# Performance work log

Measured on AMD Instinct MI355X. Metric: run time of the kernel, lower is better.

The kernel has to match this reference:

```python
import jax, jax.numpy as jnp
import numpy as np

D_MODEL = 1024
D_HID = D_MODEL // 4
N_EXPERTS = 64
TOP_K = 2


def setup_inputs() -> dict:
    key = jax.random.key(0)
    k_x, k_w1, k_b1, k_w2, k_b2 = jax.random.split(key, 5)
    # torch Linear default init: U(-1/sqrt(fan_in), 1/sqrt(fan_in))
    s1 = 1.0 / np.sqrt(D_MODEL)
    s2 = 1.0 / np.sqrt(D_HID)
    return {
        "x": jax.random.normal(k_x, (4, 4096, D_MODEL), dtype=jnp.float32),
        "W1": jax.random.uniform(k_w1, (D_MODEL, D_HID), jnp.float32, -s1, s1),
        "b1": jax.random.uniform(k_b1, (D_HID,), jnp.float32, -s1, s1),
        "W2": jax.random.uniform(k_w2, (D_HID, N_EXPERTS), jnp.float32, -s2, s2),
        "b2": jax.random.uniform(k_b2, (N_EXPERTS,), jnp.float32, -s2, s2),
    }


def reference(x, W1, b1, W2, b2):
    # gate MLP: [B,S,D] -> [B,S,H] -> tanh -> [B,S,E]
    h = jnp.tanh(jnp.einsum("bsd,dh->bsh", x, W1) + b1)
    gate_logits = jnp.einsum("bsh,he->bse", h, W2) + b2
    # top-k selection + softmax over the k selected logits
    top_logits, top_idx = jax.lax.top_k(gate_logits, TOP_K)  # [B,S,K]
    top_gates = jax.nn.softmax(top_logits, axis=-1)          # [B,S,K]
    # scatter back into dense [B,S,E] gate tensor
    onehot = jax.nn.one_hot(top_idx, N_EXPERTS, dtype=top_gates.dtype)  # [B,S,K,E]
    gates = jnp.einsum("bsk,bske->bse", top_gates, onehot)
    return gates, gate_logits
```

## Files before the change

### kernel.cpp

```cpp
#include <hip/hip_runtime.h>
#include <math.h>


#define DM 1024
#define DH 256
#define NE 64

#define W1P_OFF 0
#define W1P_STRIDE 524288
#define W2P_OFF 1572864
#define W2P_STRIDE 32768

#define HSTR 276
#define AROW 144
#define APLANE 4608
#define ABUF 13824

typedef __attribute__((ext_vector_type(8))) short bf16x8;
typedef __attribute__((ext_vector_type(4))) float f32x4;

__device__ __forceinline__ unsigned fbits(float f) { return __float_as_uint(f); }
__device__ __forceinline__ float topf(unsigned u) { return __uint_as_float(u & 0xFFFF0000u); }

__device__ __forceinline__ void split3(float v, unsigned& h, unsigned& m, unsigned& l) {
    h = fbits(v);
    float r1 = v - topf(h);
    m = fbits(r1);
    float r2 = r1 - topf(m);
    l = fbits(r2);
}
__device__ __forceinline__ unsigned packpair(unsigned a, unsigned b) {
    return (a >> 16) | (b & 0xFFFF0000u);
}
__device__ __forceinline__ bf16x8 as_bf(uint4 u) {
    union { uint4 a; bf16x8 b; } c; c.a = u; return c.b;
}

__device__ __forceinline__ void stage4(float4 f, char* wb) {
    unsigned h[4], m[4], l[4];
    split3(f.x, h[0], m[0], l[0]);
    split3(f.y, h[1], m[1], l[1]);
    split3(f.z, h[2], m[2], l[2]);
    split3(f.w, h[3], m[3], l[3]);
    uint2 dh = {packpair(h[0], h[1]), packpair(h[2], h[3])};
    uint2 dm = {packpair(m[0], m[1]), packpair(m[2], m[3])};
    uint2 dl = {packpair(l[0], l[1]), packpair(l[2], l[3])};
    *(uint2*)(wb + 0 * APLANE) = dh;
    *(uint2*)(wb + 1 * APLANE) = dm;
    *(uint2*)(wb + 2 * APLANE) = dl;
}

__device__ __forceinline__ void split_pack8(float4 f0, float4 f1,
                                            bf16x8& H, bf16x8& M, bf16x8& L) {
    float v[8] = {f0.x, f0.y, f0.z, f0.w, f1.x, f1.y, f1.z, f1.w};
    unsigned hb[8], mb[8], lb[8];
#pragma unroll
    for (int j = 0; j < 8; j++) split3(v[j], hb[j], mb[j], lb[j]);
    uint4 uh = {packpair(hb[0], hb[1]), packpair(hb[2], hb[3]),
                packpair(hb[4], hb[5]), packpair(hb[6], hb[7])};
    uint4 um = {packpair(mb[0], mb[1]), packpair(mb[2], mb[3]),
                packpair(mb[4], mb[5]), packpair(mb[6], mb[7])};
    uint4 ul = {packpair(lb[0], lb[1]), packpair(lb[2], lb[3]),
                packpair(lb[4], lb[5]), packpair(lb[6], lb[7])};
    H = as_bf(uh); M = as_bf(um); L = as_bf(ul);
}


__global__ __launch_bounds__(256)
void prep_planes(const float* __restrict__ W1, const float* __restrict__ W2,
                 char* __restrict__ ws) {
    __shared__ float tile[512];
    unsigned* w1p = (unsigned*)(ws + W1P_OFF);
    unsigned* w2p = (unsigned*)(ws + W2P_OFF);
    const int b = blockIdx.x, t = threadIdx.x;
    const int q = t & 3, L = (t >> 2) & 63;
    const int n_loc = L & 15;
    const int k_loc = ((L >> 4) & 3) * 8 + 2 * q;
    if (b < 512) {
        const int kc = b >> 4, nt = b & 15;
#pragma unroll
        for (int i = 0; i < 2; i++) {
            const int idx = t + i * 256;
            tile[idx] = W1[(size_t)(kc * 32 + (idx >> 4)) * DH + nt * 16 + (idx & 15)];
        }
        __syncthreads();
        const float v0 = tile[k_loc * 16 + n_loc];
        const float v1 = tile[(k_loc + 1) * 16 + n_loc];
        unsigned h0, m0, l0, h1, m1, l1;
        split3(v0, h0, m0, l0);
        split3(v1, h1, m1, l1);
        const int gt = b * 256 + t;
        w1p[0 * 131072 + gt] = packpair(h0, h1);
        w1p[1 * 131072 + gt] = packpair(m0, m1);
        w1p[2 * 131072 + gt] = packpair(l0, l1);
    } else {
        const int b2 = b - 512;
        const int kc = b2 >> 2, nt = b2 & 3;
#pragma unroll
        for (int i = 0; i < 2; i++) {
            const int idx = t + i * 256;
            tile[idx] = W2[(kc * 32 + (idx >> 4)) * NE + nt * 16 + (idx & 15)];
        }
        __syncthreads();
        const float v0 = tile[k_loc * 16 + n_loc];
        const float v1 = tile[(k_loc + 1) * 16 + n_loc];
        unsigned h0, m0, l0, h1, m1, l1;
        split3(v0, h0, m0, l0);
        split3(v1, h1, m1, l1);
        const int g2 = b2 * 256 + t;
        w2p[0 * 8192 + g2] = packpair(h0, h1);
        w2p[1 * 8192 + g2] = packpair(m0, m1);
        w2p[2 * 8192 + g2] = packpair(l0, l1);
    }
}

__global__ __launch_bounds__(512, 4)
void fused_gating(const float* __restrict__ x, const char* __restrict__ w1p,
                  const float* __restrict__ b1, const char* __restrict__ w2p,
                  const float* __restrict__ b2, float* __restrict__ gates,
                  float* __restrict__ logits_out) {
    __shared__ __align__(16) char alds[2 * ABUF];
    __shared__ __align__(16) float hlds[32 * HSTR];

    const int tid  = threadIdx.x;
    const int lane = tid & 63;
    const int wave = tid >> 6;
    const int m15 = lane & 15;
    const int lq  = lane >> 4;
    const int t0 = blockIdx.x * 32;

    const int stok = tid >> 4;
    const int seg  = tid & 15;
    const float* xs = x + (size_t)(t0 + stok) * DM + seg * 4;
    const int swoff = stok * AROW + seg * 8;

    const char* bbase = w1p + (size_t)(wave * 2) * 1024 + lane * 16;

    f32x4 acc[2][2];
#pragma unroll
    for (int ms = 0; ms < 2; ms++)
#pragma unroll
        for (int nt = 0; nt < 2; nt++) acc[ms][nt] = (f32x4){0.f, 0.f, 0.f, 0.f};

    stage4(*(const float4*)(xs), alds + swoff);
    float4 xc  = *(const float4*)(xs + 64);
    float4 xc2 = *(const float4*)(xs + 128);
    __syncthreads();

#pragma unroll 2
    for (int t = 0; t < 16; t++) {
        const int kcA = 2 * t, kcB = 2 * t + 1;
        uint4 b0[3][2], b1f[3][2];
#pragma unroll
        for (int p = 0; p < 3; p++)
#pragma unroll
            for (int nt = 0; nt < 2; nt++) {
                b0[p][nt]  = *(const uint4*)(bbase + p * W1P_STRIDE + kcA * 16384 + nt * 1024);
                b1f[p][nt] = *(const uint4*)(bbase + p * W1P_STRIDE + kcB * 16384 + nt * 1024);
            }
        float4 xn = *(const float4*)(xs + ((t + 3) & 15) * 64);

        const char* ab = alds + (t & 1) * ABUF + m15 * AROW + lq * 16;

        {
            const bf16x8 a0h = *(const bf16x8*)(ab + 0 * APLANE);
            const bf16x8 a0m = *(const bf16x8*)(ab + 1 * APLANE);
            const bf16x8 a0l = *(const bf16x8*)(ab + 2 * APLANE);
            const bf16x8 a1h = *(const bf16x8*)(ab + 0 * APLANE + 16 * AROW);
            const bf16x8 a1m = *(const bf16x8*)(ab + 1 * APLANE + 16 * AROW);
            const bf16x8 a1l = *(const bf16x8*)(ab + 2 * APLANE + 16 * AROW);
#pragma unroll
            for (int nt = 0; nt < 2; nt++) {
                const bf16x8 bh = as_bf(b0[0][nt]);
                const bf16x8 bm = as_bf(b0[1][nt]);
                const bf16x8 bl = as_bf(b0[2][nt]);
                f32x4 a0 = acc[0][nt];
                a0 = __builtin_amdgcn_mfma_f32_16x16x32_bf16(a0h, bh, a0, 0, 0, 0);
                a0 = __builtin_amdgcn_mfma_f32_16x16x32_bf16(a0h, bm, a0, 0, 0, 0);
                a0 = __builtin_amdgcn_mfma_f32_16x16x32_bf16(a0m, bh, a0, 0, 0, 0);
                a0 = __builtin_amdgcn_mfma_f32_16x16x32_bf16(a0h, bl, a0, 0, 0, 0);
                a0 = __builtin_amdgcn_mfma_f32_16x16x32_bf16(a0l, bh, a0, 0, 0, 0);
                a0 = __builtin_amdgcn_mfma_f32_16x16x32_bf16(a0m, bm, a0, 0, 0, 0);
                acc[0][nt] = a0;
                f32x4 a1 = acc[1][nt];
                a1 = __builtin_amdgcn_mfma_f32_16x16x32_bf16(a1h, bh, a1, 0, 0, 0);
                a1 = __builtin_amdgcn_mfma_f32_16x16x32_bf16(a1h, bm, a1, 0, 0, 0);
                a1 = __builtin_amdgcn_mfma_f32_16x16x32_bf16(a1m, bh, a1, 0, 0, 0);
                a1 = __builtin_amdgcn_mfma_f32_16x16x32_bf16(a1h, bl, a1, 0, 0, 0);
                a1 = __builtin_amdgcn_mfma_f32_16x16x32_bf16(a1l, bh, a1, 0, 0, 0);
                a1 = __builtin_amdgcn_mfma_f32_16x16x32_bf16(a1m, bm, a1, 0, 0, 0);
                acc[1][nt] = a1;
            }
        }
        {
            const bf16x8 a0h = *(const bf16x8*)(ab + 0 * APLANE + 64);
            const bf16x8 a0m = *(const bf16x8*)(ab + 1 * APLANE + 64);
            const bf16x8 a0l = *(const bf16x8*)(ab + 2 * APLANE + 64);
            const bf16x8 a1h = *(const bf16x8*)(ab + 0 * APLANE + 16 * AROW + 64);
            const bf16x8 a1m = *(const bf16x8*)(ab + 1 * APLANE + 16 * AROW + 64);
            const bf16x8 a1l = *(const bf16x8*)(ab + 2 * APLANE + 16 * AROW + 64);
#pragma unroll
            for (int nt = 0; nt < 2; nt++) {
                const bf16x8 bh = as_bf(b1f[0][nt]);
                const bf16x8 bm = as_bf(b1f[1][nt]);
                const bf16x8 bl = as_bf(b1f[2][nt]);
                f32x4 a0 = acc[0][nt];
                a0 = __builtin_amdgcn_mfma_f32_16x16x32_bf16(a0h, bh, a0, 0, 0, 0);
                a0 = __builtin_amdgcn_mfma_f32_16x16x32_bf16(a0h, bm, a0, 0, 0, 0);
                a0 = __builtin_amdgcn_mfma_f32_16x16x32_bf16(a0m, bh, a0, 0, 0, 0);
                a0 = __builtin_amdgcn_mfma_f32_16x16x32_bf16(a0h, bl, a0, 0, 0, 0);
                a0 = __builtin_amdgcn_mfma_f32_16x16x32_bf16(a0l, bh, a0, 0, 0, 0);
                a0 = __builtin_amdgcn_mfma_f32_16x16x32_bf16(a0m, bm, a0, 0, 0, 0);
                acc[0][nt] = a0;
                f32x4 a1 = acc[1][nt];
                a1 = __builtin_amdgcn_mfma_f32_16x16x32_bf16(a1h, bh, a1, 0, 0, 0);
                a1 = __builtin_amdgcn_mfma_f32_16x16x32_bf16(a1h, bm, a1, 0, 0, 0);
                a1 = __builtin_amdgcn_mfma_f32_16x16x32_bf16(a1m, bh, a1, 0, 0, 0);
                a1 = __builtin_amdgcn_mfma_f32_16x16x32_bf16(a1h, bl, a1, 0, 0, 0);
                a1 = __builtin_amdgcn_mfma_f32_16x16x32_bf16(a1l, bh, a1, 0, 0, 0);
                a1 = __builtin_amdgcn_mfma_f32_16x16x32_bf16(a1m, bm, a1, 0, 0, 0);
                acc[1][nt] = a1;
            }
        }

        stage4(xc, alds + ((t + 1) & 1) * ABUF + swoff);
        xc = xc2; xc2 = xn;
        __syncthreads();
    }

#pragma unroll
    for (int nt = 0; nt < 2; nt++) {
        const int hid = wave * 32 + nt * 16 + m15;
        const float bias = b1[hid];
#pragma unroll
        for (int ms = 0; ms < 2; ms++) {
            const int tb = ms * 16 + lq * 4;
#pragma unroll
            for (int r = 0; r < 4; r++)
                hlds[(tb + r) * HSTR + hid] = tanhf(acc[ms][nt][r] + bias);
        }
    }
    __syncthreads();

    if (wave < 2) {
        const float* hb = hlds + (wave * 16 + m15) * HSTR + lq * 8;
        const char* bt = w2p + lane * 16;

        f32x4 gacc[4];
#pragma unroll
        for (int nt = 0; nt < 4; nt++) gacc[nt] = (f32x4){0.f, 0.f, 0.f, 0.f};

#pragma unroll
        for (int kc = 0; kc < 8; kc++) {
            float4 f0 = *(const float4*)(hb + kc * 32);
            float4 f1 = *(const float4*)(hb + kc * 32 + 4);
            bf16x8 afh, afm, afl;
            split_pack8(f0, f1, afh, afm, afl);
#pragma unroll
            for (int nt = 0; nt < 4; nt++) {
                const char* tb = bt + (kc * 4 + nt) * 1024;
                bf16x8 bh = *(const bf16x8*)(tb + 0 * W2P_STRIDE);
                bf16x8 bm = *(const bf16x8*)(tb + 1 * W2P_STRIDE);
                bf16x8 bl = *(const bf16x8*)(tb + 2 * W2P_STRIDE);
                f32x4 a = gacc[nt];
                a = __builtin_amdgcn_mfma_f32_16x16x32_bf16(afh, bh, a, 0, 0, 0);
                a = __builtin_amdgcn_mfma_f32_16x16x32_bf16(afh, bm, a, 0, 0, 0);
                a = __builtin_amdgcn_mfma_f32_16x16x32_bf16(afm, bh, a, 0, 0, 0);
                a = __builtin_amdgcn_mfma_f32_16x16x32_bf16(afh, bl, a, 0, 0, 0);
                a = __builtin_amdgcn_mfma_f32_16x16x32_bf16(afl, bh, a, 0, 0, 0);
                a = __builtin_amdgcn_mfma_f32_16x16x32_bf16(afm, bm, a, 0, 0, 0);
                gacc[nt] = a;
            }
        }

        float b2v[4];
#pragma unroll
        for (int nt = 0; nt < 4; nt++) b2v[nt] = b2[nt * 16 + m15];

#pragma unroll
        for (int r = 0; r < 4; r++) {
            float v[4]; int e[4];
#pragma unroll
            for (int nt = 0; nt < 4; nt++) { v[nt] = gacc[nt][r] + b2v[nt]; e[nt] = nt * 16 + m15; }

            float a1 = v[0], a2 = v[1]; int j1 = e[0], j2 = e[1];
            if (v[1] > v[0]) { a1 = v[1]; j1 = e[1]; a2 = v[0]; j2 = e[0]; }
#pragma unroll
            for (int t = 2; t < 4; t++) {
                if (v[t] > a1) { a2 = a1; j2 = j1; a1 = v[t]; j1 = e[t]; }
                else if (v[t] > a2) { a2 = v[t]; j2 = e[t]; }
            }
#pragma unroll
            for (int off = 1; off < 16; off <<= 1) {
                float ob1 = __shfl_xor(a1, off, 64); int oj1 = __shfl_xor(j1, off, 64);
                float ob2 = __shfl_xor(a2, off, 64); int oj2 = __shfl_xor(j2, off, 64);
                bool bw = (ob1 > a1) || (ob1 == a1 && oj1 < j1);
                float w1v = bw ? ob1 : a1; int w1i = bw ? oj1 : j1;
                float lv = bw ? a1 : ob1;  int li  = bw ? j1 : oj1;
                float rv = bw ? ob2 : a2;  int ri  = bw ? oj2 : j2;
                bool cw = (lv > rv) || (lv == rv && li < ri);
                a1 = w1v; j1 = w1i;
                a2 = cw ? lv : rv; j2 = cw ? li : ri;
            }
            float ex = __expf(a2 - a1);
            float inv = 1.f / (1.f + ex);
            float g1 = inv, g2 = ex * inv;

            const size_t row = (size_t)(t0 + wave * 16 + lq * 4 + r) * NE;
#pragma unroll
            for (int nt = 0; nt < 4; nt++) {
                float gv = (e[nt] == j1) ? g1 : ((e[nt] == j2) ? g2 : 0.f);
                gates[row + e[nt]] = gv;
                logits_out[row + e[nt]] = v[nt];
            }
        }
    }
}

extern "C" void kernel_launch(void* const* d_in, const int* in_sizes, int n_in,
                              void* d_out, int out_size, void* d_ws, size_t ws_size,
                              hipStream_t stream) {
    const float* x  = (const float*)d_in[0];
    const float* W1 = (const float*)d_in[1];
    const float* b1 = (const float*)d_in[2];
    const float* W2 = (const float*)d_in[3];
    const float* b2 = (const float*)d_in[4];

    const int T = in_sizes[0] / DM;
    char* ws = (char*)d_ws;
    float* gates  = (float*)d_out;
    float* logits = (float*)d_out + (size_t)T * NE;

    prep_planes<<<512 + 32, 256, 0, stream>>>(W1, W2, ws);
    fused_gating<<<T / 32, 512, 0, stream>>>(x, ws + W1P_OFF, b1, ws + W2P_OFF, b2,
                                             gates, logits);
}
```

Baseline: 149.3 us.

## Split gating kernel into producer waves for x staging and MFMA consumer waves

Adds four producer waves (block grows from 512 to 768 threads) that load x, split each value into three bf16 planes and stage them into LDS. The eight consumer waves now only load W1 planes and run MFMAs, with s_setprio raised around the MFMA bursts. The A staging buffer and the hidden-activation buffer share one aliased LDS allocation to cut shared memory per block. The aim is to take the global-load and split work for x off the MFMA waves' critical path, at the cost of more threads per block, changed occupancy limits and producer waves idling at barriers.

```diff
diff --git a/kernel.cpp b/kernel.cpp
--- a/kernel.cpp
+++ b/kernel.cpp
@@ -15,6 +15,7 @@
 #define AROW 144
 #define APLANE 4608
 #define ABUF 13824
+#define SMEM_BYTES 35328
 
 typedef __attribute__((ext_vector_type(8))) short bf16x8;
 typedef __attribute__((ext_vector_type(4))) float f32x4;
@@ -36,18 +37,20 @@
     union { uint4 a; bf16x8 b; } c; c.a = u; return c.b;
 }
 
-__device__ __forceinline__ void stage4(float4 f, char* wb) {
-    unsigned h[4], m[4], l[4];
-    split3(f.x, h[0], m[0], l[0]);
-    split3(f.y, h[1], m[1], l[1]);
-    split3(f.z, h[2], m[2], l[2]);
-    split3(f.w, h[3], m[3], l[3]);
-    uint2 dh = {packpair(h[0], h[1]), packpair(h[2], h[3])};
-    uint2 dm = {packpair(m[0], m[1]), packpair(m[2], m[3])};
-    uint2 dl = {packpair(l[0], l[1]), packpair(l[2], l[3])};
-    *(uint2*)(wb + 0 * APLANE) = dh;
-    *(uint2*)(wb + 1 * APLANE) = dm;
-    *(uint2*)(wb + 2 * APLANE) = dl;
+__device__ __forceinline__ void stage8s(float4 f0, float4 f1, char* wb) {
+    float v[8] = {f0.x, f0.y, f0.z, f0.w, f1.x, f1.y, f1.z, f1.w};
+    unsigned hb[8], mb[8], lb[8];
+#pragma unroll
+    for (int j = 0; j < 8; j++) split3(v[j], hb[j], mb[j], lb[j]);
+    uint4 uh = {packpair(hb[0], hb[1]), packpair(hb[2], hb[3]),
+                packpair(hb[4], hb[5]), packpair(hb[6], hb[7])};
+    uint4 um = {packpair(mb[0], mb[1]), packpair(mb[2], mb[3]),
+                packpair(mb[4], mb[5]), packpair(mb[6], mb[7])};
+    uint4 ul = {packpair(lb[0], lb[1]), packpair(lb[2], lb[3]),
+                packpair(lb[4], lb[5]), packpair(lb[6], lb[7])};
+    *(uint4*)(wb + 0 * APLANE) = uh;
+    *(uint4*)(wb + 1 * APLANE) = um;
+    *(uint4*)(wb + 2 * APLANE) = ul;
 }
 
 __device__ __forceinline__ void split_pack8(float4 f0, float4 f1,
@@ -114,130 +117,148 @@
     }
 }
 
-__global__ __launch_bounds__(512, 4)
+__global__ __launch_bounds__(768, 6)
 void fused_gating(const float* __restrict__ x, const char* __restrict__ w1p,
                   const float* __restrict__ b1, const char* __restrict__ w2p,
                   const float* __restrict__ b2, float* __restrict__ gates,
                   float* __restrict__ logits_out) {
-    __shared__ __align__(16) char alds[2 * ABUF];
-    __shared__ __align__(16) float hlds[32 * HSTR];
+    __shared__ __align__(16) char smem[SMEM_BYTES];
+    char* alds = smem;
+    float* hlds = (float*)smem;
 
     const int tid  = threadIdx.x;
     const int lane = tid & 63;
     const int wave = tid >> 6;
+    const bool producer = (wave >= 8);
     const int m15 = lane & 15;
     const int lq  = lane >> 4;
     const int t0 = blockIdx.x * 32;
 
-    const int stok = tid >> 4;
-    const int seg  = tid & 15;
-    const float* xs = x + (size_t)(t0 + stok) * DM + seg * 4;
-    const int swoff = stok * AROW + seg * 8;
+    const float* xs = nullptr;
+    int swoff = 0;
+    float4 xc0, xc1;
+    if (producer) {
+        const int pt = tid - 512;
+        const int stok = pt >> 3;
+        const int seg  = pt & 7;
+        xs = x + (size_t)(t0 + stok) * DM + seg * 8;
+        swoff = stok * AROW + seg * 16;
+        stage8s(*(const float4*)(xs), *(const float4*)(xs + 4), alds + swoff);
+        xc0 = *(const float4*)(xs + 64);
+        xc1 = *(const float4*)(xs + 68);
+    }
 
     const char* bbase = w1p + (size_t)(wave * 2) * 1024 + lane * 16;
-
     f32x4 acc[2][2];
 #pragma unroll
     for (int ms = 0; ms < 2; ms++)
 #pragma unroll
         for (int nt = 0; nt < 2; nt++) acc[ms][nt] = (f32x4){0.f, 0.f, 0.f, 0.f};
 
-    stage4(*(const float4*)(xs), alds + swoff);
-    float4 xc  = *(const float4*)(xs + 64);
-    float4 xc2 = *(const float4*)(xs + 128);
     __syncthreads();
 
 #pragma unroll 2
     for (int t = 0; t < 16; t++) {
-        const int kcA = 2 * t, kcB = 2 * t + 1;
-        uint4 b0[3][2], b1f[3][2];
-#pragma unroll
-        for (int p = 0; p < 3; p++)
-#pragma unroll
-            for (int nt = 0; nt < 2; nt++) {
-                b0[p][nt]  = *(const uint4*)(bbase + p * W1P_STRIDE + kcA * 16384 + nt * 1024);
-                b1f[p][nt] = *(const uint4*)(bbase + p * W1P_STRIDE + kcB * 16384 + nt * 1024);
-            }
-        float4 xn = *(const float4*)(xs + ((t + 3) & 15) * 64);
-
-        const char* ab = alds + (t & 1) * ABUF + m15 * AROW + lq * 16;
-
-        {
-            const bf16x8 a0h = *(const bf16x8*)(ab + 0 * APLANE);
-            const bf16x8 a0m = *(const bf16x8*)(ab + 1 * APLANE);
-            const bf16x8 a0l = *(const bf16x8*)(ab + 2 * APLANE);
-            const bf16x8 a1h = *(const bf16x8*)(ab + 0 * APLANE + 16 * AROW);
-            const bf16x8 a1m = *(const bf16x8*)(ab + 1 * APLANE + 16 * AROW);
-            const bf16x8 a1l = *(const bf16x8*)(ab + 2 * APLANE + 16 * AROW);
-#pragma unroll
-            for (int nt = 0; nt < 2; nt++) {
-                const bf16x8 bh = as_bf(b0[0][nt]);
-                const bf16x8 bm = as_bf(b0[1][nt]);
-                const bf16x8 bl = as_bf(b0[2][nt]);
-                f32x4 a0 = acc[0][nt];
-                a0 = __builtin_amdgcn_mfma_f32_16x16x32_bf16(a0h, bh, a0, 0, 0, 0);
-                a0 = __builtin_amdgcn_mfma_f32_16x16x32_bf16(a0h, bm, a0, 0, 0, 0);
-                a0 = __builtin_amdgcn_mfma_f32_16x16x32_bf16(a0m, bh, a0, 0, 0, 0);
-                a0 = __builtin_amdgcn_mfma_f32_16x16x32_bf16(a0h, bl, a0, 0, 0, 0);
-                a0 = __builtin_amdgcn_mfma_f32_16x16x32_bf16(a0l, bh, a0, 0, 0, 0);
-                a0 = __builtin_amdgcn_mfma_f32_16x16x32_bf16(a0m, bm, a0, 0, 0, 0);
-                acc[0][nt] = a0;
-                f32x4 a1 = acc[1][nt];
-                a1 = __builtin_amdgcn_mfma_f32_16x16x32_bf16(a1h, bh, a1, 0, 0, 0);
-                a1 = __builtin_amdgcn_mfma_f32_16x16x32_bf16(a1h, bm, a1, 0, 0, 0);
-                a1 = __builtin_amdgcn_mfma_f32_16x16x32_bf16(a1m, bh, a1, 0, 0, 0);
-                a1 = __builtin_amdgcn_mfma_f32_16x16x32_bf16(a1h, bl, a1, 0, 0, 0);
-                a1 = __builtin_amdgcn_mfma_f32_16x16x32_bf16(a1l, bh, a1, 0, 0, 0);
-                a1 = __builtin_amdgcn_mfma_f32_16x16x32_bf16(a1m, bm, a1, 0, 0, 0);
-                acc[1][nt] = a1;
-            }
-        }
-        {
-            const bf16x8 a0h = *(const bf16x8*)(ab + 0 * APLANE + 64);
-            const bf16x8 a0m = *(const bf16x8*)(ab + 1 * APLANE + 64);
-            const bf16x8 a0l = *(const bf16x8*)(ab + 2 * APLANE + 64);
-            const bf16x8 a1h = *(const bf16x8*)(ab + 0 * APLANE + 16 * AROW + 64);
-            const bf16x8 a1m = *(const bf16x8*)(ab + 1 * APLANE + 16 * AROW + 64);
-            const bf16x8 a1l = *(const bf16x8*)(ab + 2 * APLANE + 16 * AROW + 64);
-#pragma unroll
-            for (int nt = 0; nt < 2; nt++) {
-                const bf16x8 bh = as_bf(b1f[0][nt]);
-                const bf16x8 bm = as_bf(b1f[1][nt]);
-                const bf16x8 bl = as_bf(b1f[2][nt]);
-                f32x4 a0 = acc[0][nt];
-                a0 = __builtin_amdgcn_mfma_f32_16x16x32_bf16(a0h, bh, a0, 0, 0, 0);
-                a0 = __builtin_amdgcn_mfma_f32_16x16x32_bf16(a0h, bm, a0, 0, 0, 0);
-                a0 = __builtin_amdgcn_mfma_f32_16x16x32_bf16(a0m, bh, a0, 0, 0, 0);
-                a0 = __builtin_amdgcn_mfma_f32_16x16x32_bf16(a0h, bl, a0, 0, 0, 0);
-                a0 = __builtin_amdgcn_mfma_f32_16x16x32_bf16(a0l, bh, a0, 0, 0, 0);
-                a0 = __builtin_amdgcn_mfma_f32_16x16x32_bf16(a0m, bm, a0, 0, 0, 0);
-                acc[0][nt] = a0;
-                f32x4 a1 = acc[1][nt];
-                a1 = __builtin_amdgcn_mfma_f32_16x16x32_bf16(a1h, bh, a1, 0, 0, 0);
-                a1 = __builtin_amdgcn_mfma_f32_16x16x32_bf16(a1h, bm, a1, 0, 0, 0);
-                a1 = __builtin_amdgcn_mfma_f32_16x16x32_bf16(a1m, bh, a1, 0, 0, 0);
-                a1 = __builtin_amdgcn_mfma_f32_16x16x32_bf16(a1h, bl, a1, 0, 0, 0);
-                a1 = __builtin_amdgcn_mfma_f32_16x16x32_bf16(a1l, bh, a1, 0, 0, 0);
-                a1 = __builtin_amdgcn_mfma_f32_16x16x32_bf16(a1m, bm, a1, 0, 0, 0);
-                acc[1][nt] = a1;
-            }
-        }
-
-        stage4(xc, alds + ((t + 1) & 1) * ABUF + swoff);
-        xc = xc2; xc2 = xn;
+        if (producer) {
+            const int kn = (t + 2) & 15;
+            float4 xn0 = *(const float4*)(xs + kn * 64);
+            float4 xn1 = *(const float4*)(xs + kn * 64 + 4);
+            if (t < 15)
+                stage8s(xc0, xc1, alds + ((t + 1) & 1) * ABUF + swoff);
+            xc0 = xn0; xc1 = xn1;
+        } else {
+            const int kcA = 2 * t, kcB = 2 * t + 1;
+            uint4 b0[3][2], b1f[3][2];
+#pragma unroll
+            for (int p = 0; p < 3; p++)
+#pragma unroll
+                for (int nt = 0; nt < 2; nt++) {
+                    b0[p][nt]  = *(const uint4*)(bbase + p * W1P_STRIDE + kcA * 16384 + nt * 1024);
+                    b1f[p][nt] = *(const uint4*)(bbase + p * W1P_STRIDE + kcB * 16384 + nt * 1024);
+                }
+
+            const char* ab = alds + (t & 1) * ABUF + m15 * AROW + lq * 16;
+
+            {
+                const bf16x8 a0h = *(const bf16x8*)(ab + 0 * APLANE);
+                const bf16x8 a0m = *(const bf16x8*)(ab + 1 * APLANE);
+                const bf16x8 a0l = *(const bf16x8*)(ab + 2 * APLANE);
+                const bf16x8 a1h = *(const bf16x8*)(ab + 0 * APLANE + 16 * AROW);
+                const bf16x8 a1m = *(const bf16x8*)(ab + 1 * APLANE + 16 * AROW);
+                const bf16x8 a1l = *(const bf16x8*)(ab + 2 * APLANE + 16 * AROW);
+                __builtin_amdgcn_s_setprio(1);
+#pragma unroll
+                for (int nt = 0; nt < 2; nt++) {
+                    const bf16x8 bh = as_bf(b0[0][nt]);
+                    const bf16x8 bm = as_bf(b0[1][nt]);
+                    const bf16x8 bl = as_bf(b0[2][nt]);
+                    f32x4 a0 = acc[0][nt];
+                    a0 = __builtin_amdgcn_mfma_f32_16x16x32_bf16(a0h, bh, a0, 0, 0, 0);
+                    a0 = __builtin_amdgcn_mfma_f32_16x16x32_bf16(a0h, bm, a0, 0, 0, 0);
+                    a0 = __builtin_amdgcn_mfma_f32_16x16x32_bf16(a0m, bh, a0, 0, 0, 0);
+                    a0 = __builtin_amdgcn_mfma_f32_16x16x32_bf16(a0h, bl, a0, 0, 0, 0);
+                    a0 = __builtin_amdgcn_mfma_f32_16x16x32_bf16(a0l, bh, a0, 0, 0, 0);
+                    a0 = __builtin_amdgcn_mfma_f32_16x16x32_bf16(a0m, bm, a0, 0, 0, 0);
+                    acc[0][nt] = a0;
+                    f32x4 a1 = acc[1][nt];
+                    a1 = __builtin_amdgcn_mfma_f32_16x16x32_bf16(a1h, bh, a1, 0, 0, 0);
+                    a1 = __builtin_amdgcn_mfma_f32_16x16x32_bf16(a1h, bm, a1, 0, 0, 0);
+                    a1 = __builtin_amdgcn_mfma_f32_16x16x32_bf16(a1m, bh, a1, 0, 0, 0);
+                    a1 = __builtin_amdgcn_mfma_f32_16x16x32_bf16(a1h, bl, a1, 0, 0, 0);
+                    a1 = __builtin_amdgcn_mfma_f32_16x16x32_bf16(a1l, bh, a1, 0, 0, 0);
+                    a1 = __builtin_amdgcn_mfma_f32_16x16x32_bf16(a1m, bm, a1, 0, 0, 0);
+                    acc[1][nt] = a1;
+                }
+                __builtin_amdgcn_s_setprio(0);
+            }
+            {
+                const bf16x8 a0h = *(const bf16x8*)(ab + 0 * APLANE + 64);
+                const bf16x8 a0m = *(const bf16x8*)(ab + 1 * APLANE + 64);
+                const bf16x8 a0l = *(const bf16x8*)(ab + 2 * APLANE + 64);
+                const bf16x8 a1h = *(const bf16x8*)(ab + 0 * APLANE + 16 * AROW + 64);
+                const bf16x8 a1m = *(const bf16x8*)(ab + 1 * APLANE + 16 * AROW + 64);
+                const bf16x8 a1l = *(const bf16x8*)(ab + 2 * APLANE + 16 * AROW + 64);
+                __builtin_amdgcn_s_setprio(1);
+#pragma unroll
+                for (int nt = 0; nt < 2; nt++) {
+                    const bf16x8 bh = as_bf(b1f[0][nt]);
+                    const bf16x8 bm = as_bf(b1f[1][nt]);
+                    const bf16x8 bl = as_bf(b1f[2][nt]);
+                    f32x4 a0 = acc[0][nt];
+                    a0 = __builtin_amdgcn_mfma_f32_16x16x32_bf16(a0h, bh, a0, 0, 0, 0);
+                    a0 = __builtin_amdgcn_mfma_f32_16x16x32_bf16(a0h, bm, a0, 0, 0, 0);
+                    a0 = __builtin_amdgcn_mfma_f32_16x16x32_bf16(a0m, bh, a0, 0, 0, 0);
+                    a0 = __builtin_amdgcn_mfma_f32_16x16x32_bf16(a0h, bl, a0, 0, 0, 0);
+                    a0 = __builtin_amdgcn_mfma_f32_16x16x32_bf16(a0l, bh, a0, 0, 0, 0);
+                    a0 = __builtin_amdgcn_mfma_f32_16x16x32_bf16(a0m, bm, a0, 0, 0, 0);
+                    acc[0][nt] = a0;
+                    f32x4 a1 = acc[1][nt];
+                    a1 = __builtin_amdgcn_mfma_f32_16x16x32_bf16(a1h, bh, a1, 0, 0, 0);
+                    a1 = __builtin_amdgcn_mfma_f32_16x16x32_bf16(a1h, bm, a1, 0, 0, 0);
+                    a1 = __builtin_amdgcn_mfma_f32_16x16x32_bf16(a1m, bh, a1, 0, 0, 0);
+                    a1 = __builtin_amdgcn_mfma_f32_16x16x32_bf16(a1h, bl, a1, 0, 0, 0);
+                    a1 = __builtin_amdgcn_mfma_f32_16x16x32_bf16(a1l, bh, a1, 0, 0, 0);
+                    a1 = __builtin_amdgcn_mfma_f32_16x16x32_bf16(a1m, bm, a1, 0, 0, 0);
+                    acc[1][nt] = a1;
+                }
+                __builtin_amdgcn_s_setprio(0);
+            }
+        }
         __syncthreads();
     }
 
-#pragma unroll
-    for (int nt = 0; nt < 2; nt++) {
-        const int hid = wave * 32 + nt * 16 + m15;
-        const float bias = b1[hid];
-#pragma unroll
-        for (int ms = 0; ms < 2; ms++) {
-            const int tb = ms * 16 + lq * 4;
-#pragma unroll
-            for (int r = 0; r < 4; r++)
-                hlds[(tb + r) * HSTR + hid] = tanhf(acc[ms][nt][r] + bias);
+    if (!producer) {
+#pragma unroll
+        for (int nt = 0; nt < 2; nt++) {
+            const int hid = wave * 32 + nt * 16 + m15;
+            const float bias = b1[hid];
+#pragma unroll
+            for (int ms = 0; ms < 2; ms++) {
+                const int tb = ms * 16 + lq * 4;
+#pragma unroll
+                for (int r = 0; r < 4; r++)
+                    hlds[(tb + r) * HSTR + hid] = tanhf(acc[ms][nt][r] + bias);
+            }
         }
     }
     __syncthreads();
@@ -286,9 +307,9 @@
             float a1 = v[0], a2 = v[1]; int j1 = e[0], j2 = e[1];
             if (v[1] > v[0]) { a1 = v[1]; j1 = e[1]; a2 = v[0]; j2 = e[0]; }
 #pragma unroll
-            for (int t = 2; t < 4; t++) {
-                if (v[t] > a1) { a2 = a1; j2 = j1; a1 = v[t]; j1 = e[t]; }
-                else if (v[t] > a2) { a2 = v[t]; j2 = e[t]; }
+            for (int tt = 2; tt < 4; tt++) {
+                if (v[tt] > a1) { a2 = a1; j2 = j1; a1 = v[tt]; j1 = e[tt]; }
+                else if (v[tt] > a2) { a2 = v[tt]; j2 = e[tt]; }
             }
 #pragma unroll
             for (int off = 1; off < 16; off <<= 1) {
@@ -332,6 +353,6 @@
     float* logits = (float*)d_out + (size_t)T * NE;
 
     prep_planes<<<512 + 32, 256, 0, stream>>>(W1, W2, ws);
-    fused_gating<<<T / 32, 512, 0, stream>>>(x, ws + W1P_OFF, b1, ws + W2P_OFF, b2,
+    fused_gating<<<T / 32, 768, 0, stream>>>(x, ws + W1P_OFF, b1, ws + W2P_OFF, b2,
                                              gates, logits);
 }
```

New measurement: 266.9 us. 78.7% more time.
